# Kernel optimization log

Hardware: AMD Instinct MI355X
Metric: run time of the kernel (lower is better)

The kernel has to match this reference:

```python
import jax, jax.numpy as jnp
import numpy as np
import math

NUM_HEADS = 16
D_KV = 64
D_MODEL = 1024
NUM_BUCKETS = 32
MAX_DISTANCE = 128
SEQ = 2048
BATCH = 2


def _relative_position_bucket(relative_position):
    # bidirectional T5 bucketing
    num_buckets = NUM_BUCKETS // 2  # 16
    buckets = (relative_position > 0).astype(jnp.int32) * num_buckets
    rp = jnp.abs(relative_position)
    max_exact = num_buckets // 2  # 8
    is_small = rp < max_exact
    rp_safe = jnp.maximum(rp, 1)  # avoid log(0); masked by is_small anyway
    rp_large = max_exact + (
        jnp.log(rp_safe.astype(jnp.float32) / max_exact)
        / math.log(MAX_DISTANCE / max_exact)
        * (num_buckets - max_exact)
    ).astype(jnp.int32)
    rp_large = jnp.minimum(rp_large, num_buckets - 1)
    return buckets + jnp.where(is_small, rp, rp_large)


def _position_bias(rel_bias_table, q_len, k_len):
    ctx = jnp.arange(q_len)[:, None]
    mem = jnp.arange(k_len)[None, :]
    buckets = _relative_position_bucket(mem - ctx)  # (q,k)
    vals = rel_bias_table[buckets]  # (q,k,h)
    return jnp.transpose(vals, (2, 0, 1))[None]  # (1,h,q,k)


def setup_inputs() -> dict:
    key = jax.random.key(0)
    ks = jax.random.split(key, 6)
    s = 1.0 / math.sqrt(D_MODEL)
    return {
        "hidden_states": jax.random.normal(ks[0], (BATCH, SEQ, D_MODEL), jnp.float32),
        "Wq": jax.random.normal(ks[1], (D_MODEL, NUM_HEADS * D_KV), jnp.float32) * s,
        "Wk": jax.random.normal(ks[2], (D_MODEL, NUM_HEADS * D_KV), jnp.float32) * s,
        "Wv": jax.random.normal(ks[3], (D_MODEL, NUM_HEADS * D_KV), jnp.float32) * s,
        "Wo": jax.random.normal(ks[4], (NUM_HEADS * D_KV, D_MODEL), jnp.float32) * s,
        "rel_bias_table": jax.random.normal(ks[5], (NUM_BUCKETS, NUM_HEADS), jnp.float32),
    }


def reference(hidden_states, Wq, Wk, Wv, Wo, rel_bias_table):
    b, s, _ = hidden_states.shape
    q = (hidden_states @ Wq).reshape(b, s, NUM_HEADS, D_KV).transpose(0, 2, 1, 3)
    k = (hidden_states @ Wk).reshape(b, s, NUM_HEADS, D_KV).transpose(0, 2, 1, 3)
    v = (hidden_states @ Wv).reshape(b, s, NUM_HEADS, D_KV).transpose(0, 2, 1, 3)
    # T5: NO query scaling, additive relative-position bias
    scores = jnp.einsum("bhqd,bhkd->bhqk", q, k) + _position_bias(rel_bias_table, s, s)
    attn = jax.nn.softmax(scores, axis=-1)  # dropout is identity in eval
    out = jnp.einsum("bhqk,bhkd->bhqd", attn, v)
    out = out.transpose(0, 2, 1, 3).reshape(b, s, NUM_HEADS * D_KV)
    return out @ Wo
```

## Files before the change

kernel.cpp:

```cpp
#include <hip/hip_runtime.h>
#include <hip/hip_bf16.h>
#include <math.h>

#define NUM_HEADS 16
#define D_KV 64
#define D_MODEL 1024
#define SEQ 2048
#define BATCH 2
#define LOG2E 1.4426950408889634f

using bf16x8 = __attribute__((ext_vector_type(8))) short;
using bf16x4 = __attribute__((ext_vector_type(4))) short;
using f32x4  = __attribute__((ext_vector_type(4))) float;

__device__ inline unsigned short f2bf(float f) {
  union { float f; unsigned int i; } v; v.f = f;
  unsigned int u = v.i;
  return (unsigned short)((u + 0x7FFFu + ((u >> 16) & 1u)) >> 16);
}
__device__ inline unsigned short f2bf_fast(float f) {
  union { float f; unsigned int i; } v; v.f = f;
  return (unsigned short)((v.i + 0x8000u) >> 16);
}

#if __has_builtin(__builtin_amdgcn_exp2f)
#define EXP2(x) __builtin_amdgcn_exp2f(x)
#else
#define EXP2(x) __expf((x) * 0.6931471805599453f)
#endif

__device__ inline unsigned int pk_bf16(float a, float b) {
#if __has_builtin(__builtin_amdgcn_cvt_pk_bf16_f32)
  auto v = __builtin_amdgcn_cvt_pk_bf16_f32(a, b);
  unsigned int u; __builtin_memcpy(&u, &v, 4);
  return u;
#else
  return ((unsigned int)f2bf_fast(b) << 16) | f2bf_fast(a);
#endif
}

__device__ inline void gld_lds16(const unsigned short* g, unsigned short* l) {
  __builtin_amdgcn_global_load_lds(
      (const __attribute__((address_space(1))) unsigned int*)g,
      (__attribute__((address_space(3))) unsigned int*)l, 16, 0, 0);
}

__global__ __launch_bounds__(256) void prep_kernel(const float* __restrict__ X,
                                                   const float* __restrict__ W0,
                                                   const float* __restrict__ W1,
                                                   const float* __restrict__ W2,
                                                   const float* __restrict__ W3,
                                                   const float* __restrict__ tbl,
                                                   unsigned short* __restrict__ xbf,
                                                   unsigned short* __restrict__ wt,
                                                   float* __restrict__ biasF) {
  __shared__ __align__(16) unsigned short T[64][72];
  int bid = blockIdx.x;
  int t = threadIdx.x;
  if (bid < 2048) {
    int i = (bid * 256 + t) * 8;
    __align__(16) unsigned short tmp[8];
#pragma unroll
    for (int e = 0; e < 8; e++) tmp[e] = f2bf(X[i + e]);
    *(uint4*)&xbf[i] = *(uint4*)tmp;
  } else if (bid < 3072) {
    int rem = bid - 2048;
    int z = rem >> 8, tid = rem & 255;
    const float* in = (z == 0) ? W0 : (z == 1) ? W1 : (z == 2) ? W2 : W3;
    unsigned short* o = wt + (long)z * 1048576;
    int r0 = (tid & 15) * 64, c0 = (tid >> 4) * 64;
#pragma unroll
    for (int i = 0; i < 2; i++) {
      int c = t + 256 * i; int r = c >> 3, k8 = (c & 7) * 8;
      const float* src = &in[(long)(r0 + r) * 1024 + c0 + k8];
      __align__(16) unsigned short tmp[8];
#pragma unroll
      for (int e = 0; e < 8; e++) tmp[e] = f2bf(src[e]);
      *(uint4*)&T[r][k8] = *(uint4*)tmp;
    }
    __syncthreads();
#pragma unroll
    for (int i = 0; i < 2; i++) {
      int c = t + 256 * i; int r = c >> 3, k8 = (c & 7) * 8;
      __align__(16) unsigned short tmp[8];
#pragma unroll
      for (int e = 0; e < 8; e++) tmp[e] = T[k8 + e][r];
      *(uint4*)&o[(long)(c0 + r) * 1024 + r0 + k8] = *(uint4*)tmp;
    }
  } else {
#pragma unroll
    for (int ii = 0; ii < 16; ii++) {
      int idx = t + 256 * ii;
      if (idx >= 4095) break;
      int rel = idx - 2047;
      int bucket = (rel > 0) ? 16 : 0;
      int rp = rel < 0 ? -rel : rel;
      int add;
      if (rp < 8) add = rp;
      else {
        int rl = 8 + (int)(logf((float)rp * 0.125f) / logf(16.0f) * 8.0f);
        add = rl < 15 ? rl : 15;
      }
      bucket += add;
#pragma unroll
      for (int h = 0; h < 16; h++) biasF[h * 4096 + idx] = tbl[bucket * 16 + h] * LOG2E;
    }
  }
}

__global__ __launch_bounds__(256) void gemm_kernel(const unsigned short* __restrict__ X,
                                                   const unsigned short* __restrict__ Wt,
                                                   unsigned short* __restrict__ out_b,
                                                   unsigned short* __restrict__ out_vt) {
  __shared__ __align__(16) unsigned short SMEM[128 * 136];
  unsigned short* As = SMEM;
  unsigned short* Bs = SMEM + 128 * 32;
  const int K = 1024;
  int m0 = blockIdx.x * 128;
  int n0 = blockIdx.y * 128;
  const unsigned short* W = Wt + (long)blockIdx.z * 1048576;
  unsigned short* outq = out_b + (long)blockIdx.z * 4194304;
  float scale = (blockIdx.z == 0) ? LOG2E : 1.0f;
  int t = threadIdx.x;
  int w = t >> 6, l = t & 63;
  int wr = (w >> 1) * 64, wc = (w & 1) * 64;
  int lr = l & 15, lq = l >> 4;
  f32x4 acc[4][4];
#pragma unroll
  for (int i = 0; i < 4; i++)
#pragma unroll
    for (int j = 0; j < 4; j++) acc[i][j] = (f32x4){0.f, 0.f, 0.f, 0.f};

  for (int k0 = 0; k0 < K; k0 += 32) {
#pragma unroll
    for (int i = 0; i < 2; i++) {
      int c = t + 256 * i;
      int r = c >> 2, kc = (c & 3) * 8;
      gld_lds16(&X[(long)(m0 + r) * K + k0 + kc], &As[c * 8]);
      gld_lds16(&W[(long)(n0 + r) * K + k0 + kc], &Bs[c * 8]);
    }
    __syncthreads();
    bf16x8 a[4], b[4];
#pragma unroll
    for (int mi = 0; mi < 4; mi++) a[mi] = *(const bf16x8*)&As[(wr + mi * 16 + lr) * 32 + lq * 8];
#pragma unroll
    for (int ni = 0; ni < 4; ni++) b[ni] = *(const bf16x8*)&Bs[(wc + ni * 16 + lr) * 32 + lq * 8];
#pragma unroll
    for (int mi = 0; mi < 4; mi++)
#pragma unroll
      for (int ni = 0; ni < 4; ni++)
        acc[mi][ni] = __builtin_amdgcn_mfma_f32_16x16x32_bf16(a[mi], b[ni], acc[mi][ni], 0, 0, 0);
    __syncthreads();
  }

  if (blockIdx.z == 2) {
    unsigned short* Cs = SMEM;
#pragma unroll
    for (int mi = 0; mi < 4; mi++)
#pragma unroll
      for (int ni = 0; ni < 4; ni++) {
        int nl = wc + ni * 16 + lr;
        int ml = wr + mi * 16 + lq * 4;
        unsigned int s0 = pk_bf16(acc[mi][ni][0], acc[mi][ni][1]);
        unsigned int s1 = pk_bf16(acc[mi][ni][2], acc[mi][ni][3]);
        *(uint2*)&Cs[nl * 136 + ml] = (uint2){s0, s1};
      }
    __syncthreads();
    int b2 = m0 >> 11, sbase = m0 & 2047;
#pragma unroll
    for (int i = 0; i < 8; i++) {
      int c = t + 256 * i;
      int row = c >> 4, ch = c & 15;
      uint4 v = *(const uint4*)&Cs[row * 136 + ch * 8];
      int n = n0 + row, h = n >> 6, d = n & 63;
      *(uint4*)&out_vt[(((long)(b2 * 16 + h) * 64 + d) << 11) + sbase + ch * 8] = v;
    }
  } else {
    unsigned short* Cs = SMEM;
#pragma unroll
    for (int mi = 0; mi < 4; mi++)
#pragma unroll
      for (int ni = 0; ni < 4; ni++)
#pragma unroll
        for (int r = 0; r < 4; r++)
          Cs[(wr + mi * 16 + lq * 4 + r) * 136 + wc + ni * 16 + lr] = f2bf(acc[mi][ni][r] * scale);
    __syncthreads();
    int b2 = m0 >> 11, sbase = m0 & 2047;
#pragma unroll
    for (int i = 0; i < 8; i++) {
      int c = t + 256 * i;
      int row = c >> 4, ch = c & 15;
      uint4 v = *(const uint4*)&Cs[row * 136 + ch * 8];
      int n = n0 + ch * 8, h = n >> 6, d = n & 63;
      *(uint4*)&outq[((long)(b2 * 16 + h) * 2048 + sbase + row) * 64 + d] = v;
    }
  }
}

__global__ __launch_bounds__(256) void ogemm_kernel(const unsigned short* __restrict__ X,
                                                    const unsigned short* __restrict__ W,
                                                    float* __restrict__ out) {
  __shared__ __align__(16) unsigned char SMEM[64 * 68 * 4];
  unsigned short* As = (unsigned short*)SMEM;
  unsigned short* Bs = As + 4096;
  float* Csf = (float*)SMEM;
  const int K = 1024;
  int m0 = blockIdx.x * 64;
  int n0 = blockIdx.y * 64;
  int t = threadIdx.x;
  int w = t >> 6, l = t & 63;
  int wr = (w >> 1) * 32, wc = (w & 1) * 32;
  int lr = l & 15, lq = l >> 4;
  f32x4 acc[2][2];
#pragma unroll
  for (int i = 0; i < 2; i++)
#pragma unroll
    for (int j = 0; j < 2; j++) acc[i][j] = (f32x4){0.f, 0.f, 0.f, 0.f};

  for (int k0 = 0; k0 < K; k0 += 64) {
#pragma unroll
    for (int i = 0; i < 2; i++) {
      int c = t + 256 * i;
      int p = c >> 8, r = (c >> 2) & 63, kc = (c & 3) * 8;
      gld_lds16(&X[(long)(m0 + r) * K + k0 + p * 32 + kc], &As[c * 8]);
      gld_lds16(&W[(long)(n0 + r) * K + k0 + p * 32 + kc], &Bs[c * 8]);
    }
    __syncthreads();
    bf16x8 a[2][2], b[2][2];
#pragma unroll
    for (int ks = 0; ks < 2; ks++) {
#pragma unroll
      for (int mi = 0; mi < 2; mi++) a[mi][ks] = *(const bf16x8*)&As[ks * 2048 + (wr + mi * 16 + lr) * 32 + lq * 8];
#pragma unroll
      for (int ni = 0; ni < 2; ni++) b[ni][ks] = *(const bf16x8*)&Bs[ks * 2048 + (wc + ni * 16 + lr) * 32 + lq * 8];
    }
#pragma unroll
    for (int ks = 0; ks < 2; ks++)
#pragma unroll
      for (int mi = 0; mi < 2; mi++)
#pragma unroll
        for (int ni = 0; ni < 2; ni++)
          acc[mi][ni] = __builtin_amdgcn_mfma_f32_16x16x32_bf16(a[mi][ks], b[ni][ks], acc[mi][ni], 0, 0, 0);
    __syncthreads();
  }

#pragma unroll
  for (int mi = 0; mi < 2; mi++)
#pragma unroll
    for (int ni = 0; ni < 2; ni++)
#pragma unroll
      for (int r = 0; r < 4; r++)
        Csf[(wr + mi * 16 + lq * 4 + r) * 68 + wc + ni * 16 + lr] = acc[mi][ni][r];
  __syncthreads();
#pragma unroll
  for (int i = 0; i < 4; i++) {
    int c = t + 256 * i;
    int row = c >> 4, ch = c & 15;
    float4 v = *(const float4*)&Csf[row * 68 + ch * 4];
    *(float4*)&out[(long)(m0 + row) * 1024 + n0 + ch * 4] = v;
  }
}

__global__ __launch_bounds__(512) void attn_kernel(const unsigned short* __restrict__ Q,
                                                   const unsigned short* __restrict__ Km,
                                                   const unsigned short* __restrict__ Vt,
                                                   const float* __restrict__ biasF,
                                                   unsigned short* __restrict__ O) {
  __shared__ __align__(16) unsigned short KV[4][4608];
  __shared__ __align__(16) float biasRf[2][2176];
  int q0 = blockIdx.x * 128;
  int bh = blockIdx.y;
  int b_ = bh >> 4, h = bh & 15;
  const unsigned short* Qb = Q  + (long)bh * SEQ * 64;
  const unsigned short* Kb = Km + (long)bh * SEQ * 64;
  const unsigned short* Vb = Vt + (long)bh * 64 * SEQ;
  const float* btabF = biasF + h * 4096;
  int t = threadIdx.x;
  int w = t >> 6, l = t & 63;
  int g = w >> 2, wg = w & 3;
  int lr = l & 15, lq = l >> 4;
  int qw = wg * 32;

  float bL = btabF[0], bH = btabF[4094];

  int gbase = 1920 - q0;
  for (int i = t; i < 2176; i += 512) {
    int g0 = gbase + i;     if (g0 > 4094) g0 = 4094;
    int g1 = gbase + i + 1; if (g1 > 4094) g1 = 4094;
    biasRf[0][i] = btabF[g0];
    biasRf[1][i] = btabF[g1];
  }

  bf16x8 aq[2][2];
#pragma unroll
  for (int qt = 0; qt < 2; qt++)
#pragma unroll
    for (int ks = 0; ks < 2; ks++)
      aq[qt][ks] = *(const bf16x8*)&Qb[(long)(q0 + qw + qt * 16 + lr) * 64 + ks * 32 + lq * 8];

  int rs = t >> 3, fs = (t & 7) * 8;

  uint4 kpa = *(const uint4*)&Kb[(long)rs * 64 + fs];
  uint4 kpb = *(const uint4*)&Kb[(long)(64 + rs) * 64 + fs];
  uint4 vpa = *(const uint4*)&Vb[(long)rs * SEQ + fs];
  uint4 vpb = *(const uint4*)&Vb[(long)rs * SEQ + 64 + fs];
  *(uint4*)&KV[0][rs * 72 + fs] = kpa;
  *(uint4*)&KV[1][rs * 72 + fs] = kpb;
  *(uint4*)&KV[2][rs * 72 + fs] = vpa;
  *(uint4*)&KV[3][rs * 72 + fs] = vpb;

  f32x4 accO[4][2];
  float rsum[2] = {0.f, 0.f};
#pragma unroll
  for (int qt = 0; qt < 2; qt++)
#pragma unroll
    for (int dt = 0; dt < 4; dt++) accO[dt][qt] = (f32x4){0.f, 0.f, 0.f, 0.f};

  int vb = 127 + lq * 4 - qw - lr;
  int bj2 = vb & 1;
  const float* brow = biasRf[bj2];
  int pbc = vb - bj2 - 16;

  for (int i = 0; i < 16; i++) {
    __syncthreads();
    int k0 = (2 * i + g) * 64;
    bool more = i < 15;

    float2 bbl[5][2];
    int dq = k0 - q0;
    if (dq >= 218 || dq <= -154) {
      float bc = (dq >= 218) ? bH : bL;
      float2 bc2 = (float2){bc, bc};
#pragma unroll
      for (int m = 0; m < 5; m++) { bbl[m][0] = bc2; bbl[m][1] = bc2; }
    } else {
      int pb = pbc + k0;
#pragma unroll
      for (int m = 0; m < 5; m++) {
        bbl[m][0] = *(const float2*)&brow[pb + 16 * m];
        bbl[m][1] = *(const float2*)&brow[pb + 16 * m + 2];
      }
    }

    bf16x8 bk[4][2];
#pragma unroll
    for (int kt = 0; kt < 4; kt++)
#pragma unroll
      for (int ks = 0; ks < 2; ks++)
        bk[kt][ks] = *(const bf16x8*)&KV[g][(kt * 16 + lr) * 72 + ks * 32 + lq * 8];

    if (more) {
      const unsigned short* Kn = Kb + (long)(2 * i + 2) * 64 * 64;
      const unsigned short* Vn = Vb + (2 * i + 2) * 64;
      kpa = *(const uint4*)&Kn[(long)rs * 64 + fs];
      kpb = *(const uint4*)&Kn[(long)(64 + rs) * 64 + fs];
      vpa = *(const uint4*)&Vn[(long)rs * SEQ + fs];
      vpb = *(const uint4*)&Vn[(long)rs * SEQ + 64 + fs];
    }

    f32x4 sacc[4][2];
#pragma unroll
    for (int kt = 0; kt < 4; kt++)
#pragma unroll
      for (int qt = 0; qt < 2; qt++) sacc[kt][qt] = (f32x4){0.f, 0.f, 0.f, 0.f};
#pragma unroll
    for (int ks = 0; ks < 2; ks++)
#pragma unroll
      for (int kt = 0; kt < 4; kt++)
#pragma unroll
        for (int qt = 0; qt < 2; qt++)
          sacc[kt][qt] = __builtin_amdgcn_mfma_f32_16x16x32_bf16(bk[kt][ks], aq[qt][ks], sacc[kt][qt], 0, 0, 0);

#pragma unroll
    for (int ktp = 0; ktp < 2; ktp++) {
      bf16x8 va8[4];
#pragma unroll
      for (int dt = 0; dt < 4; dt++) {
        const unsigned short* vp = &KV[2 + g][(dt * 16 + lr) * 72 + ktp * 32 + lq * 4];
        bf16x4 vlo = *(const bf16x4*)vp;
        bf16x4 vhi = *(const bf16x4*)(vp + 16);
        va8[dt] = __builtin_shufflevector(vlo, vhi, 0, 1, 2, 3, 4, 5, 6, 7);
      }
#pragma unroll
      for (int qt = 0; qt < 2; qt++) {
        unsigned int u[4];
#pragma unroll
        for (int kth = 0; kth < 2; kth++) {
          int kt = ktp * 2 + kth;
          int blk = kt - qt + 1;
          float p0 = EXP2(sacc[kt][qt][0] + bbl[blk][0].x);
          float p1 = EXP2(sacc[kt][qt][1] + bbl[blk][0].y);
          float p2 = EXP2(sacc[kt][qt][2] + bbl[blk][1].x);
          float p3 = EXP2(sacc[kt][qt][3] + bbl[blk][1].y);
          rsum[qt] += (p0 + p1) + (p2 + p3);
          u[kth * 2]     = pk_bf16(p0, p1);
          u[kth * 2 + 1] = pk_bf16(p2, p3);
        }
        union { unsigned int uu[4]; bf16x8 v; } pbu;
        pbu.uu[0] = u[0]; pbu.uu[1] = u[1]; pbu.uu[2] = u[2]; pbu.uu[3] = u[3];
#pragma unroll
        for (int dt = 0; dt < 4; dt++)
          accO[dt][qt] = __builtin_amdgcn_mfma_f32_16x16x32_bf16(va8[dt], pbu.v, accO[dt][qt], 0, 0, 0);
      }
    }

    __syncthreads();
    if (more) {
      *(uint4*)&KV[0][rs * 72 + fs] = kpa;
      *(uint4*)&KV[1][rs * 72 + fs] = kpb;
      *(uint4*)&KV[2][rs * 72 + fs] = vpa;
      *(uint4*)&KV[3][rs * 72 + fs] = vpb;
    }
  }

#pragma unroll
  for (int qt = 0; qt < 2; qt++) {
    rsum[qt] += __shfl_xor(rsum[qt], 16);
    rsum[qt] += __shfl_xor(rsum[qt], 32);
  }

  float* mrg = (float*)&KV[0][0];
  int slot = (wg * 64 + l) * 34;
  if (g == 1) {
    float2* mp = (float2*)&mrg[slot];
    int j = 0;
#pragma unroll
    for (int dt = 0; dt < 4; dt++)
#pragma unroll
      for (int qt = 0; qt < 2; qt++) {
        mp[j++] = (float2){accO[dt][qt][0], accO[dt][qt][1]};
        mp[j++] = (float2){accO[dt][qt][2], accO[dt][qt][3]};
      }
    mp[16] = (float2){rsum[0], rsum[1]};
  }
  __syncthreads();
  if (g == 0) {
    const float2* mp = (const float2*)&mrg[slot];
    int j = 0;
#pragma unroll
    for (int dt = 0; dt < 4; dt++)
#pragma unroll
      for (int qt = 0; qt < 2; qt++) {
        float2 a = mp[j++], b2 = mp[j++];
        accO[dt][qt][0] += a.x;  accO[dt][qt][1] += a.y;
        accO[dt][qt][2] += b2.x; accO[dt][qt][3] += b2.y;
      }
    float2 ls = mp[16];
    float rl0 = 1.0f / (rsum[0] + ls.x);
    float rl1 = 1.0f / (rsum[1] + ls.y);
#pragma unroll
    for (int qt = 0; qt < 2; qt++) {
      float rl = qt ? rl1 : rl0;
      int q = q0 + qw + qt * 16 + lr;
#pragma unroll
      for (int dt = 0; dt < 4; dt++) {
        unsigned int s0 = ((unsigned int)f2bf(accO[dt][qt][1] * rl) << 16) | f2bf(accO[dt][qt][0] * rl);
        unsigned int s1 = ((unsigned int)f2bf(accO[dt][qt][3] * rl) << 16) | f2bf(accO[dt][qt][2] * rl);
        *(uint2*)&O[((long)(b_ * SEQ + q)) * 1024 + h * 64 + dt * 16 + lq * 4] = (uint2){s0, s1};
      }
    }
  }
}

extern "C" void kernel_launch(void* const* d_in, const int* in_sizes, int n_in,
                              void* d_out, int out_size, void* d_ws, size_t ws_size,
                              hipStream_t stream) {
  const float* X   = (const float*)d_in[0];
  const float* Wq  = (const float*)d_in[1];
  const float* Wk  = (const float*)d_in[2];
  const float* Wv  = (const float*)d_in[3];
  const float* Wo  = (const float*)d_in[4];
  const float* tbl = (const float*)d_in[5];

  unsigned short* wt    = (unsigned short*)d_ws;
  unsigned short* xbf   = wt + 4 * 1048576;
  unsigned short* q_ws  = xbf + 4194304;
  unsigned short* k_ws  = q_ws + 4194304;
  unsigned short* vt_ws = k_ws + 4194304;
  float* biasF = (float*)(vt_ws + 4194304);
  unsigned short* o_ws  = xbf;

  prep_kernel<<<3073, 256, 0, stream>>>(X, Wq, Wk, Wv, Wo, tbl, xbf, wt, biasF);
  gemm_kernel<<<dim3(32, 8, 3), 256, 0, stream>>>(xbf, wt, q_ws, vt_ws);
  attn_kernel<<<dim3(16, 32), 512, 0, stream>>>(q_ws, k_ws, vt_ws, biasF, o_ws);
  ogemm_kernel<<<dim3(64, 16), 256, 0, stream>>>(o_ws, wt + 3 * 1048576, (float*)d_out);
}
```

Before: 205.8 us.

## Deepen GEMM K-step, enlarge output GEMM tile, add MFMA priority hints and packed softmax math

The QKV GEMM now loads a 64-wide K slice per iteration instead of 32, halving the number of barriers per tile. The output GEMM uses 128x64 tiles with a two-pass LDS epilogue, giving more reuse per block but launching half as many blocks. The attention kernel wraps its MFMA sections in s_setprio hints and does the bias add and row-sum accumulation as packed two-wide float vectors. Costs are more LDS and registers per block, fewer output GEMM blocks to fill the GPU, and an extra barrier in the epilogue.

Result: slower. 211.3 us (+2.7%).

```diff
diff --git a/kernel.cpp b/kernel.cpp
--- a/kernel.cpp
+++ b/kernel.cpp
@@ -12,6 +12,7 @@
 using bf16x8 = __attribute__((ext_vector_type(8))) short;
 using bf16x4 = __attribute__((ext_vector_type(4))) short;
 using f32x4  = __attribute__((ext_vector_type(4))) float;
+using f32x2  = __attribute__((ext_vector_type(2))) float;
 
 __device__ inline unsigned short f2bf(float f) {
   union { float f; unsigned int i; } v; v.f = f;
@@ -114,7 +115,7 @@
                                                    unsigned short* __restrict__ out_vt) {
   __shared__ __align__(16) unsigned short SMEM[128 * 136];
   unsigned short* As = SMEM;
-  unsigned short* Bs = SMEM + 128 * 32;
+  unsigned short* Bs = SMEM + 8192;
   const int K = 1024;
   int m0 = blockIdx.x * 128;
   int n0 = blockIdx.y * 128;
@@ -131,25 +132,30 @@
 #pragma unroll
     for (int j = 0; j < 4; j++) acc[i][j] = (f32x4){0.f, 0.f, 0.f, 0.f};
 
-  for (int k0 = 0; k0 < K; k0 += 32) {
-#pragma unroll
-    for (int i = 0; i < 2; i++) {
+  for (int k0 = 0; k0 < K; k0 += 64) {
+#pragma unroll
+    for (int i = 0; i < 4; i++) {
       int c = t + 256 * i;
-      int r = c >> 2, kc = (c & 3) * 8;
-      gld_lds16(&X[(long)(m0 + r) * K + k0 + kc], &As[c * 8]);
-      gld_lds16(&W[(long)(n0 + r) * K + k0 + kc], &Bs[c * 8]);
-    }
-    __syncthreads();
-    bf16x8 a[4], b[4];
-#pragma unroll
-    for (int mi = 0; mi < 4; mi++) a[mi] = *(const bf16x8*)&As[(wr + mi * 16 + lr) * 32 + lq * 8];
-#pragma unroll
-    for (int ni = 0; ni < 4; ni++) b[ni] = *(const bf16x8*)&Bs[(wc + ni * 16 + lr) * 32 + lq * 8];
-#pragma unroll
-    for (int mi = 0; mi < 4; mi++)
-#pragma unroll
-      for (int ni = 0; ni < 4; ni++)
-        acc[mi][ni] = __builtin_amdgcn_mfma_f32_16x16x32_bf16(a[mi], b[ni], acc[mi][ni], 0, 0, 0);
+      int p = c >> 9, r = (c >> 2) & 127, kc = (c & 3) * 8;
+      gld_lds16(&X[(long)(m0 + r) * K + k0 + p * 32 + kc], &As[c * 8]);
+      gld_lds16(&W[(long)(n0 + r) * K + k0 + p * 32 + kc], &Bs[c * 8]);
+    }
+    __syncthreads();
+    bf16x8 a[4][2], b[4][2];
+#pragma unroll
+    for (int ks = 0; ks < 2; ks++) {
+#pragma unroll
+      for (int mi = 0; mi < 4; mi++) a[mi][ks] = *(const bf16x8*)&As[ks * 4096 + (wr + mi * 16 + lr) * 32 + lq * 8];
+#pragma unroll
+      for (int ni = 0; ni < 4; ni++) b[ni][ks] = *(const bf16x8*)&Bs[ks * 4096 + (wc + ni * 16 + lr) * 32 + lq * 8];
+    }
+#pragma unroll
+    for (int ks = 0; ks < 2; ks++)
+#pragma unroll
+      for (int mi = 0; mi < 4; mi++)
+#pragma unroll
+        for (int ni = 0; ni < 4; ni++)
+          acc[mi][ni] = __builtin_amdgcn_mfma_f32_16x16x32_bf16(a[mi][ks], b[ni][ks], acc[mi][ni], 0, 0, 0);
     __syncthreads();
   }
 
@@ -200,44 +206,49 @@
 __global__ __launch_bounds__(256) void ogemm_kernel(const unsigned short* __restrict__ X,
                                                     const unsigned short* __restrict__ W,
                                                     float* __restrict__ out) {
-  __shared__ __align__(16) unsigned char SMEM[64 * 68 * 4];
+  __shared__ __align__(16) unsigned char SMEM[24576];
   unsigned short* As = (unsigned short*)SMEM;
-  unsigned short* Bs = As + 4096;
+  unsigned short* Bs = As + 8192;
   float* Csf = (float*)SMEM;
   const int K = 1024;
-  int m0 = blockIdx.x * 64;
+  int m0 = blockIdx.x * 128;
   int n0 = blockIdx.y * 64;
   int t = threadIdx.x;
   int w = t >> 6, l = t & 63;
-  int wr = (w >> 1) * 32, wc = (w & 1) * 32;
+  int wr = (w >> 1) * 64, wc = (w & 1) * 32;
   int lr = l & 15, lq = l >> 4;
-  f32x4 acc[2][2];
-#pragma unroll
-  for (int i = 0; i < 2; i++)
+  f32x4 acc[4][2];
+#pragma unroll
+  for (int i = 0; i < 4; i++)
 #pragma unroll
     for (int j = 0; j < 2; j++) acc[i][j] = (f32x4){0.f, 0.f, 0.f, 0.f};
 
   for (int k0 = 0; k0 < K; k0 += 64) {
+#pragma unroll
+    for (int i = 0; i < 4; i++) {
+      int c = t + 256 * i;
+      int p = c >> 9, r = (c >> 2) & 127, kc = (c & 3) * 8;
+      gld_lds16(&X[(long)(m0 + r) * K + k0 + p * 32 + kc], &As[c * 8]);
+    }
 #pragma unroll
     for (int i = 0; i < 2; i++) {
       int c = t + 256 * i;
       int p = c >> 8, r = (c >> 2) & 63, kc = (c & 3) * 8;
-      gld_lds16(&X[(long)(m0 + r) * K + k0 + p * 32 + kc], &As[c * 8]);
       gld_lds16(&W[(long)(n0 + r) * K + k0 + p * 32 + kc], &Bs[c * 8]);
     }
     __syncthreads();
-    bf16x8 a[2][2], b[2][2];
+    bf16x8 a[4][2], b[2][2];
 #pragma unroll
     for (int ks = 0; ks < 2; ks++) {
 #pragma unroll
-      for (int mi = 0; mi < 2; mi++) a[mi][ks] = *(const bf16x8*)&As[ks * 2048 + (wr + mi * 16 + lr) * 32 + lq * 8];
+      for (int mi = 0; mi < 4; mi++) a[mi][ks] = *(const bf16x8*)&As[ks * 4096 + (wr + mi * 16 + lr) * 32 + lq * 8];
 #pragma unroll
       for (int ni = 0; ni < 2; ni++) b[ni][ks] = *(const bf16x8*)&Bs[ks * 2048 + (wc + ni * 16 + lr) * 32 + lq * 8];
     }
 #pragma unroll
     for (int ks = 0; ks < 2; ks++)
 #pragma unroll
-      for (int mi = 0; mi < 2; mi++)
+      for (int mi = 0; mi < 4; mi++)
 #pragma unroll
         for (int ni = 0; ni < 2; ni++)
           acc[mi][ni] = __builtin_amdgcn_mfma_f32_16x16x32_bf16(a[mi][ks], b[ni][ks], acc[mi][ni], 0, 0, 0);
@@ -245,19 +256,25 @@
   }
 
 #pragma unroll
-  for (int mi = 0; mi < 2; mi++)
-#pragma unroll
-    for (int ni = 0; ni < 2; ni++)
-#pragma unroll
-      for (int r = 0; r < 4; r++)
-        Csf[(wr + mi * 16 + lq * 4 + r) * 68 + wc + ni * 16 + lr] = acc[mi][ni][r];
-  __syncthreads();
-#pragma unroll
-  for (int i = 0; i < 4; i++) {
-    int c = t + 256 * i;
-    int row = c >> 4, ch = c & 15;
-    float4 v = *(const float4*)&Csf[row * 68 + ch * 4];
-    *(float4*)&out[(long)(m0 + row) * 1024 + n0 + ch * 4] = v;
+  for (int p = 0; p < 2; p++) {
+    if (p) __syncthreads();
+    if ((w >> 1) == p) {
+#pragma unroll
+      for (int mi = 0; mi < 4; mi++)
+#pragma unroll
+        for (int ni = 0; ni < 2; ni++)
+#pragma unroll
+          for (int r = 0; r < 4; r++)
+            Csf[(mi * 16 + lq * 4 + r) * 68 + wc + ni * 16 + lr] = acc[mi][ni][r];
+    }
+    __syncthreads();
+#pragma unroll
+    for (int i = 0; i < 4; i++) {
+      int c = t + 256 * i;
+      int row = c >> 4, ch = c & 15;
+      float4 v = *(const float4*)&Csf[row * 68 + ch * 4];
+      *(float4*)&out[(long)(m0 + p * 64 + row) * 1024 + n0 + ch * 4] = v;
+    }
   }
 }
 
@@ -310,7 +327,7 @@
   *(uint4*)&KV[3][rs * 72 + fs] = vpb;
 
   f32x4 accO[4][2];
-  float rsum[2] = {0.f, 0.f};
+  f32x2 rsum2[2] = {(f32x2){0.f, 0.f}, (f32x2){0.f, 0.f}};
 #pragma unroll
   for (int qt = 0; qt < 2; qt++)
 #pragma unroll
@@ -326,19 +343,19 @@
     int k0 = (2 * i + g) * 64;
     bool more = i < 15;
 
-    float2 bbl[5][2];
+    f32x2 bbl[5][2];
     int dq = k0 - q0;
     if (dq >= 218 || dq <= -154) {
       float bc = (dq >= 218) ? bH : bL;
-      float2 bc2 = (float2){bc, bc};
+      f32x2 bc2 = (f32x2){bc, bc};
 #pragma unroll
       for (int m = 0; m < 5; m++) { bbl[m][0] = bc2; bbl[m][1] = bc2; }
     } else {
       int pb = pbc + k0;
 #pragma unroll
       for (int m = 0; m < 5; m++) {
-        bbl[m][0] = *(const float2*)&brow[pb + 16 * m];
-        bbl[m][1] = *(const float2*)&brow[pb + 16 * m + 2];
+        bbl[m][0] = *(const f32x2*)&brow[pb + 16 * m];
+        bbl[m][1] = *(const f32x2*)&brow[pb + 16 * m + 2];
       }
     }
 
@@ -363,6 +380,7 @@
     for (int kt = 0; kt < 4; kt++)
 #pragma unroll
       for (int qt = 0; qt < 2; qt++) sacc[kt][qt] = (f32x4){0.f, 0.f, 0.f, 0.f};
+    __builtin_amdgcn_s_setprio(1);
 #pragma unroll
     for (int ks = 0; ks < 2; ks++)
 #pragma unroll
@@ -370,6 +388,7 @@
 #pragma unroll
         for (int qt = 0; qt < 2; qt++)
           sacc[kt][qt] = __builtin_amdgcn_mfma_f32_16x16x32_bf16(bk[kt][ks], aq[qt][ks], sacc[kt][qt], 0, 0, 0);
+    __builtin_amdgcn_s_setprio(0);
 
 #pragma unroll
     for (int ktp = 0; ktp < 2; ktp++) {
@@ -388,19 +407,23 @@
         for (int kth = 0; kth < 2; kth++) {
           int kt = ktp * 2 + kth;
           int blk = kt - qt + 1;
-          float p0 = EXP2(sacc[kt][qt][0] + bbl[blk][0].x);
-          float p1 = EXP2(sacc[kt][qt][1] + bbl[blk][0].y);
-          float p2 = EXP2(sacc[kt][qt][2] + bbl[blk][1].x);
-          float p3 = EXP2(sacc[kt][qt][3] + bbl[blk][1].y);
-          rsum[qt] += (p0 + p1) + (p2 + p3);
+          f32x2 s01 = __builtin_shufflevector(sacc[kt][qt], sacc[kt][qt], 0, 1) + bbl[blk][0];
+          f32x2 s23 = __builtin_shufflevector(sacc[kt][qt], sacc[kt][qt], 2, 3) + bbl[blk][1];
+          float p0 = EXP2(s01.x);
+          float p1 = EXP2(s01.y);
+          float p2 = EXP2(s23.x);
+          float p3 = EXP2(s23.y);
+          rsum2[qt] += (f32x2){p0, p1} + (f32x2){p2, p3};
           u[kth * 2]     = pk_bf16(p0, p1);
           u[kth * 2 + 1] = pk_bf16(p2, p3);
         }
         union { unsigned int uu[4]; bf16x8 v; } pbu;
         pbu.uu[0] = u[0]; pbu.uu[1] = u[1]; pbu.uu[2] = u[2]; pbu.uu[3] = u[3];
+        __builtin_amdgcn_s_setprio(1);
 #pragma unroll
         for (int dt = 0; dt < 4; dt++)
           accO[dt][qt] = __builtin_amdgcn_mfma_f32_16x16x32_bf16(va8[dt], pbu.v, accO[dt][qt], 0, 0, 0);
+        __builtin_amdgcn_s_setprio(0);
       }
     }
 
@@ -413,6 +436,7 @@
     }
   }
 
+  float rsum[2] = {rsum2[0].x + rsum2[0].y, rsum2[1].x + rsum2[1].y};
 #pragma unroll
   for (int qt = 0; qt < 2; qt++) {
     rsum[qt] += __shfl_xor(rsum[qt], 16);
@@ -483,5 +507,5 @@
   prep_kernel<<<3073, 256, 0, stream>>>(X, Wq, Wk, Wv, Wo, tbl, xbf, wt, biasF);
   gemm_kernel<<<dim3(32, 8, 3), 256, 0, stream>>>(xbf, wt, q_ws, vt_ws);
   attn_kernel<<<dim3(16, 32), 512, 0, stream>>>(q_ws, k_ws, vt_ws, biasF, o_ws);
-  ogemm_kernel<<<dim3(64, 16), 256, 0, stream>>>(o_ws, wt + 3 * 1048576, (float*)d_out);
-}
+  ogemm_kernel<<<dim3(32, 16), 256, 0, stream>>>(o_ws, wt + 3 * 1048576, (float*)d_out);
+}
```
